# Kernel optimization log

Measured on AMD Instinct MI355X. Metric: run time of the kernel, lower is better.

Reference implementation:

```python
import jax, jax.numpy as jnp
import numpy as np

EPS = 1e-5
HEADS = 16
HEAD_DIM = 64
SIG_SCALE = HEAD_DIM ** (-0.25)
DEFAULT_BIAS = -3.0

def layernorm(x, scale, offset):
    mu = jnp.mean(x, axis=-1, keepdims=True)
    var = jnp.mean(jnp.square(x - mu), axis=-1, keepdims=True)
    return (x - mu) * jax.lax.rsqrt(var + EPS) * scale + offset

def setup_inputs() -> dict:
    key = jax.random.key(0)
    ks = jax.random.split(key, 16)
    B, Nq, Nk, D, A = 2, 2048, 2048, 1024, 1024
    s = 0.02
    return {
        "query_feats": jax.random.normal(ks[0], (B, Nq, D), jnp.float32),
        "key_feats": jax.random.normal(ks[1], (B, Nk, D), jnp.float32),
        "Wq": jax.random.normal(ks[2], (A, D), jnp.float32) * s,
        "Wk": jax.random.normal(ks[3], (A, D), jnp.float32) * s,
        "Wv": jax.random.normal(ks[4], (A, D), jnp.float32) * s,
        "Wo": jax.random.normal(ks[5], (D, A), jnp.float32) * s,
        "qn_scale": jnp.ones((HEAD_DIM,), jnp.float32),
        "qn_bias": jnp.zeros((HEAD_DIM,), jnp.float32),
        "kn_scale": jnp.ones((HEAD_DIM,), jnp.float32),
        "kn_bias": jnp.zeros((HEAD_DIM,), jnp.float32),
        "ln_q_scale": jnp.ones((D,), jnp.float32),
        "ln_q_bias": jnp.zeros((D,), jnp.float32),
        "ln_out_scale": jnp.ones((D,), jnp.float32),
        "ln_out_bias": jnp.zeros((D,), jnp.float32),
        "gamma": jnp.full((D,), 1e-5, jnp.float32),
    }

def reference(query_feats, key_feats, Wq, Wk, Wv, Wo, qn_scale, qn_bias, kn_scale, kn_bias, ln_q_scale, ln_q_bias, ln_out_scale, ln_out_bias, gamma):
    B, Nq, _ = query_feats.shape
    Nk = key_feats.shape[1]
    residual = query_feats
    xq = layernorm(query_feats, ln_q_scale, ln_q_bias)  # norm_first
    # projections (torch Linear: x @ W.T)
    q = (xq @ Wq.T).reshape(B, Nq, HEADS, HEAD_DIM).transpose(0, 2, 1, 3)
    k = (key_feats @ Wk.T).reshape(B, Nk, HEADS, HEAD_DIM).transpose(0, 2, 1, 3)
    v = (key_feats @ Wv.T).reshape(B, Nk, HEADS, HEAD_DIM).transpose(0, 2, 1, 3)
    # qk-norm over head_dim, then fixed sigmoid scale
    q = layernorm(q, qn_scale, qn_bias) * SIG_SCALE
    k = layernorm(k, kn_scale, kn_bias) * SIG_SCALE
    scores = jnp.einsum('bhqd,bhkd->bhqk', q, k) + DEFAULT_BIAS
    # hardware-optimized sigmoid: 0.5*(1+tanh(0.5*x))
    attn = 0.5 * (1.0 + jnp.tanh(0.5 * scores))
    ctx = jnp.einsum('bhqk,bhkd->bhqd', attn, v)
    ctx = ctx.transpose(0, 2, 1, 3).reshape(B, Nq, HEADS * HEAD_DIM)
    out = ctx @ Wo.T
    out = gamma * out
    out = residual + out
    out = layernorm(out, ln_out_scale, ln_out_bias)  # post_norm
    return out
```

## Files before the change

kernel.cpp:

```cpp
#include <hip/hip_runtime.h>

typedef unsigned short u16;
typedef unsigned int u32;
typedef __bf16 bf16x8 __attribute__((ext_vector_type(8)));
typedef float f32x4 __attribute__((ext_vector_type(4)));
typedef float f32x16 __attribute__((ext_vector_type(16)));
typedef u16 u16x8 __attribute__((ext_vector_type(8)));
typedef u16 u16x4 __attribute__((ext_vector_type(4)));
typedef u32 u32x4 __attribute__((ext_vector_type(4)));

#define LN_EPS 1e-5f
#define SIG_SCALE_F 0.35355339059327379f
#define NLOG2E -1.4426950408889634f
#define BIAS_L2E 4.328085122666891f

__device__ __forceinline__ u16 f2bf(float f) {
    u32 u = __builtin_bit_cast(u32, f);
    u32 r = u + 0x7fffu + ((u >> 16) & 1u);
    return (u16)(r >> 16);
}
__device__ __forceinline__ float bf2f(u16 v) {
    return __builtin_bit_cast(float, (u32)v << 16);
}
__device__ __forceinline__ u32 pk_hi(float a, float b) {
    return __builtin_amdgcn_perm(__builtin_bit_cast(u32, b), __builtin_bit_cast(u32, a),
                                 0x07060302u);
}

__device__ __forceinline__ void gload16(const u16* g, u16* lds) {
    __builtin_amdgcn_global_load_lds(
        (const __attribute__((address_space(1))) u32*)g,
        (__attribute__((address_space(3))) u32*)lds, 16, 0, 0);
}

__device__ __forceinline__ void gemm_core(f32x4 acc[4][4],
                                          const u16* __restrict__ A, const u16* __restrict__ B,
                                          int Kiter, int lda, int ldb,
                                          long m0, long n0, u16* As, u16* Bs) {
    const int tid = threadIdx.x;
    const int lane = tid & 63;
    const int wave = tid >> 6;
    const int r15 = lane & 15;
    const int qd = lane >> 4;
    const int wm = (wave >> 1) * 64;
    const int wn = (wave & 1) * 64;

    const int srow = wave * 16 + (lane >> 2);
    const int c0 = (lane & 3) ^ (srow & 3);
    const u16* Ap0 = A + (m0 + srow) * lda + c0 * 8;
    const u16* Ap1 = A + (m0 + srow + 64) * lda + c0 * 8;
    const u16* Bp0 = B + (n0 + srow) * ldb + c0 * 8;
    const u16* Bp1 = B + (n0 + srow + 64) * ldb + c0 * 8;
    u16* As0 = As + wave * 512;
    u16* As1 = As + (wave + 4) * 512;
    u16* Bs0 = Bs + wave * 512;
    u16* Bs1 = Bs + (wave + 4) * 512;

    for (int kt = 0; kt < Kiter; kt += 32) {
        __syncthreads();
        gload16(Ap0 + kt, As0);
        gload16(Ap1 + kt, As1);
        gload16(Bp0 + kt, Bs0);
        gload16(Bp1 + kt, Bs1);
        __syncthreads();
        bf16x8 af[4], bfr[4];
#pragma unroll
        for (int i = 0; i < 4; i++) {
            int row = wm + i * 16 + r15;
            af[i] = *(const bf16x8*)(As + row * 32 + ((qd ^ (row & 3)) * 8));
        }
#pragma unroll
        for (int j = 0; j < 4; j++) {
            int row = wn + j * 16 + r15;
            bfr[j] = *(const bf16x8*)(Bs + row * 32 + ((qd ^ (row & 3)) * 8));
        }
#pragma unroll
        for (int i = 0; i < 4; i++)
#pragma unroll
            for (int j = 0; j < 4; j++)
                acc[i][j] = __builtin_amdgcn_mfma_f32_16x16x32_bf16(af[i], bfr[j], acc[i][j], 0, 0, 0);
    }
}

__global__ __launch_bounds__(256, 3) void gemm_qkv(const u16* __restrict__ xq, const u16* __restrict__ keyb,
                                                   const u16* __restrict__ Wqb, const u16* __restrict__ Wkb,
                                                   const u16* __restrict__ Wvb,
                                                   const float* __restrict__ qns, const float* __restrict__ qnb,
                                                   const float* __restrict__ kns, const float* __restrict__ knb,
                                                   u16* __restrict__ qln, u16* __restrict__ kln,
                                                   u16* __restrict__ vt) {
    __shared__ __attribute__((aligned(16))) u16 As[128 * 32];
    __shared__ __attribute__((aligned(16))) u16 Bs[128 * 32];
    const int z = blockIdx.z;
    const u16* A = (z == 0) ? xq : keyb;
    const u16* B = (z == 0) ? Wqb : ((z == 1) ? Wkb : Wvb);
    const long m0 = (long)blockIdx.x * 128;
    const long n0 = (long)blockIdx.y * 128;

    f32x4 acc[4][4];
#pragma unroll
    for (int i = 0; i < 4; i++)
#pragma unroll
        for (int j = 0; j < 4; j++) acc[i][j] = (f32x4){0.f, 0.f, 0.f, 0.f};

    gemm_core(acc, A, B, 1024, 1024, 1024, m0, n0, As, Bs);

    const int lane = threadIdx.x & 63;
    const int wave = threadIdx.x >> 6;
    const int r15 = lane & 15;
    const int qd = lane >> 4;
    const int wm = (wave >> 1) * 64;
    const int wn = (wave & 1) * 64;

    if (z <= 1) {
        u16* C = (z == 0) ? qln : kln;
        const float* sc_ = (z == 0) ? qns : kns;
        const float* bs_ = (z == 0) ? qnb : knb;
        float scl[4], bia[4];
#pragma unroll
        for (int j = 0; j < 4; j++) {
            scl[j] = sc_[j * 16 + r15] * SIG_SCALE_F;
            bia[j] = bs_[j * 16 + r15] * SIG_SCALE_F;
        }
#pragma unroll
        for (int i = 0; i < 4; i++) {
#pragma unroll
            for (int rr = 0; rr < 4; rr++) {
                float a0 = acc[i][0][rr], a1 = acc[i][1][rr], a2 = acc[i][2][rr], a3 = acc[i][3][rr];
                float s1 = (a0 + a1) + (a2 + a3);
                float s2 = __builtin_fmaf(a3, a3,
                           __builtin_fmaf(a2, a2, __builtin_fmaf(a1, a1, a0 * a0)));
#pragma unroll
                for (int off = 1; off <= 8; off <<= 1) {
                    s1 += __shfl_xor(s1, off, 64);
                    s2 += __shfl_xor(s2, off, 64);
                }
                float mu = s1 * (1.0f / 64.0f);
                float var = __builtin_fmaf(-mu, mu, s2 * (1.0f / 64.0f));
                float rs = rsqrtf(var + LN_EPS);
                long row = m0 + wm + i * 16 + qd * 4 + rr;
#pragma unroll
                for (int j = 0; j < 4; j++) {
                    long col = n0 + wn + j * 16 + r15;
                    float o = __builtin_fmaf((acc[i][j][rr] - mu) * rs, scl[j], bia[j]);
                    C[row * 1024 + col] = f2bf(o);
                }
            }
        }
    } else {
#pragma unroll
        for (int i = 0; i < 4; i++)
#pragma unroll
            for (int rr = 0; rr < 4; rr++) {
                int grow = (int)(m0 + wm + i * 16 + qd * 4 + rr);
                int bb = grow >> 11;
                int kk = grow & 2047;
#pragma unroll
                for (int j = 0; j < 4; j++) {
                    int col = (int)(n0 + wn + j * 16 + r15);
                    int hh = col >> 6;
                    int dd = col & 63;
                    vt[((size_t)(bb * 16 + hh) * 64 + dd) * 2048 + kk] = f2bf(acc[i][j][rr]);
                }
            }
    }
}

__global__ __launch_bounds__(256, 4) void gemm_o(const u16* __restrict__ ctx, const u16* __restrict__ Wob,
                                                 u16* __restrict__ opre) {
    __shared__ __attribute__((aligned(16))) u16 As[128 * 32];
    __shared__ __attribute__((aligned(16))) u16 Bs[128 * 32];
    const int z = blockIdx.z;
    const int koff = z * 256;
    u16* C = opre + (size_t)z * 4194304;
    const long m0 = (long)blockIdx.x * 128;
    const long n0 = (long)blockIdx.y * 128;
    f32x4 acc[4][4];
#pragma unroll
    for (int i = 0; i < 4; i++)
#pragma unroll
        for (int j = 0; j < 4; j++) acc[i][j] = (f32x4){0.f, 0.f, 0.f, 0.f};
    gemm_core(acc, ctx + koff, Wob + koff, 256, 1024, 1024, m0, n0, As, Bs);

    const int lane = threadIdx.x & 63;
    const int wave = threadIdx.x >> 6;
    const int r15 = lane & 15;
    const int qd = lane >> 4;
    const int wm = (wave >> 1) * 64;
    const int wn = (wave & 1) * 64;
#pragma unroll
    for (int i = 0; i < 4; i++)
#pragma unroll
        for (int rr = 0; rr < 4; rr++) {
            long row = m0 + wm + i * 16 + qd * 4 + rr;
#pragma unroll
            for (int j = 0; j < 4; j++)
                C[row * 1024 + n0 + wn + j * 16 + r15] = f2bf(acc[i][j][rr]);
        }
}

__device__ __forceinline__ bf16x8 frag64(const u16* base, int row, int kidx) {
    return *(const bf16x8*)(base + row * 64 + ((kidx ^ (row & 7)) * 8));
}

__global__ __launch_bounds__(512, 4) void attn_sigmoid_v7(const u16* __restrict__ q,
                                                          const u16* __restrict__ k,
                                                          const u16* __restrict__ vt,
                                                          u16* __restrict__ ctx) {
    __shared__ __attribute__((aligned(16))) u16 Sh[8192 + 8192 + 8192];
    u16* Qs = Sh;
    u16* Ks = Sh + 8192;
    u16* Vs = Sh + 16384;
    float* Obuf = (float*)(Sh + 8192);

    const int tid = threadIdx.x;
    const int lane = tid & 63;
    const int wave = tid >> 6;
    const int l31 = lane & 31;
    const int h = lane >> 5;
    const int qsub = wave & 3;
    const int kh = wave >> 2;
    const int hd = blockIdx.x;
    const int q0 = blockIdx.y * 128;
    const int b = blockIdx.z;
    const int bh = b * 16 + hd;

    const int lr0 = lane >> 3;
    const int lc0 = lane & 7;
    {
#pragma unroll
        for (int i = 0; i < 2; i++) {
            int s = wave * 2 + i;
            int row = s * 8 + lr0;
            int c = lc0 ^ (row & 7);
            gload16(q + (size_t)(b * 2048 + q0 + row) * 1024 + hd * 64 + c * 8, Qs + s * 512);
        }
    }
    __syncthreads();
    bf16x8 qB[4];
#pragma unroll
    for (int dblk = 0; dblk < 4; dblk++)
        qB[dblk] = frag64(Qs, qsub * 32 + l31, dblk * 2 + h);

    f32x16 accO[2];
#pragma unroll
    for (int dt = 0; dt < 2; dt++)
#pragma unroll
        for (int r = 0; r < 16; r++) accO[dt][r] = 0.f;

    u16* Ksh = Ks + kh * 4096;
    u16* Vsh = Vs + kh * 4096;
    const int wsub = wave & 3;
    const int kbeg = kh * 1024;
    for (int kc = kbeg; kc < kbeg + 1024; kc += 64) {
        __syncthreads();
#pragma unroll
        for (int i = 0; i < 2; i++) {
            int s = wsub * 2 + i;
            int row = s * 8 + lr0;
            int c = lc0 ^ (row & 7);
            gload16(k + (size_t)(b * 2048 + kc + row) * 1024 + hd * 64 + c * 8, Ksh + s * 512);
            gload16(vt + (size_t)(bh * 64 + row) * 2048 + kc + c * 8, Vsh + s * 512);
        }
        __syncthreads();

        f32x16 accS[2];
#pragma unroll
        for (int mt = 0; mt < 2; mt++) {
#pragma unroll
            for (int r = 0; r < 16; r++) accS[mt][r] = 0.f;
#pragma unroll
            for (int dblk = 0; dblk < 4; dblk++) {
                bf16x8 aK = frag64(Ksh, mt * 32 + l31, dblk * 2 + h);
                accS[mt] = __builtin_amdgcn_mfma_f32_32x32x16_bf16(aK, qB[dblk], accS[mt], 0, 0, 0);
            }
        }

        u32 pg[2][4][2];
#pragma unroll
        for (int mt = 0; mt < 2; mt++)
#pragma unroll
            for (int g = 0; g < 4; g++) {
                float p[4];
#pragma unroll
                for (int e = 0; e < 4; e++) {
                    float t = __builtin_fmaf(accS[mt][g * 4 + e], NLOG2E, BIAS_L2E);
                    float u = __builtin_amdgcn_exp2f(t);
                    p[e] = __builtin_amdgcn_rcpf(1.0f + u);
                }
                pg[mt][g][0] = pk_hi(p[0], p[1]);
                pg[mt][g][1] = pk_hi(p[2], p[3]);
            }

#pragma unroll
        for (int mt = 0; mt < 2; mt++)
#pragma unroll
            for (int kblk = 0; kblk < 2; kblk++) {
                int glo = kblk * 2, ghi = kblk * 2 + 1;
                u32 x0 = (u32)__shfl_xor((int)pg[mt][glo][0], 32, 64);
                u32 x1 = (u32)__shfl_xor((int)pg[mt][glo][1], 32, 64);
                u32 y0 = (u32)__shfl_xor((int)pg[mt][ghi][0], 32, 64);
                u32 y1 = (u32)__shfl_xor((int)pg[mt][ghi][1], 32, 64);
                u32x4 fr;
                fr[0] = h ? y0 : pg[mt][glo][0];
                fr[1] = h ? y1 : pg[mt][glo][1];
                fr[2] = h ? pg[mt][ghi][0] : x0;
                fr[3] = h ? pg[mt][ghi][1] : x1;
                bf16x8 aP = __builtin_bit_cast(bf16x8, fr);
#pragma unroll
                for (int dt = 0; dt < 2; dt++) {
                    bf16x8 bV = frag64(Vsh, dt * 32 + l31, mt * 4 + kblk * 2 + h);
                    accO[dt] = __builtin_amdgcn_mfma_f32_32x32x16_bf16(aP, bV, accO[dt], 0, 0, 0);
                }
            }
    }

    __syncthreads();
    if (kh == 1) {
#pragma unroll
        for (int dt = 0; dt < 2; dt++)
#pragma unroll
            for (int r = 0; r < 16; r++) {
                int ql = qsub * 32 + (r & 3) + 8 * (r >> 2) + 4 * h;
                Obuf[ql * 64 + dt * 32 + l31] = accO[dt][r];
            }
    }
    __syncthreads();
    if (kh == 0) {
#pragma unroll
        for (int dt = 0; dt < 2; dt++)
#pragma unroll
            for (int r = 0; r < 16; r++) {
                int ql = qsub * 32 + (r & 3) + 8 * (r >> 2) + 4 * h;
                float s = accO[dt][r] + Obuf[ql * 64 + dt * 32 + l31];
                ctx[(size_t)(b * 2048 + q0 + ql) * 1024 + hd * 64 + dt * 32 + l31] = f2bf(s);
            }
    }
}

__global__ __launch_bounds__(256) void prep(const float* __restrict__ w0, const float* __restrict__ w1,
                                            const float* __restrict__ w2, const float* __restrict__ w3,
                                            const float* __restrict__ kf, const float* __restrict__ qf,
                                            const float* __restrict__ lnq_s, const float* __restrict__ lnq_b,
                                            u16* __restrict__ wdst, u16* __restrict__ kdst,
                                            u16* __restrict__ xq) {
    const int bx = blockIdx.x;
    const int tid = threadIdx.x;
    if (bx < 6144) {
        size_t e = ((size_t)bx * 256 + tid) * 4;
        const float* src;
        u16* dst;
        if (e < 4194304) {
            src = ((e >> 20) == 0 ? w0 : (e >> 20) == 1 ? w1 : (e >> 20) == 2 ? w2 : w3) + (e & 1048575);
            dst = wdst + e;
        } else {
            size_t off = e - 4194304;
            src = kf + off;
            dst = kdst + off;
        }
        float4 xv = *(const float4*)src;
        u16x4 o;
        o[0] = f2bf(xv.x);
        o[1] = f2bf(xv.y);
        o[2] = f2bf(xv.z);
        o[3] = f2bf(xv.w);
        *(u16x4*)dst = o;
    } else {
        __shared__ float s1buf[4], s2buf[4];
        const int row = bx - 6144;
        const size_t base = (size_t)row * 1024 + tid * 4;
        const float4 xv = *(const float4*)(qf + base);
        float s1 = xv.x + xv.y + xv.z + xv.w;
        float s2 = xv.x * xv.x + xv.y * xv.y + xv.z * xv.z + xv.w * xv.w;
        int lane = tid & 63, wave = tid >> 6;
#pragma unroll
        for (int off = 32; off > 0; off >>= 1) {
            s1 += __shfl_down(s1, off, 64);
            s2 += __shfl_down(s2, off, 64);
        }
        if (lane == 0) { s1buf[wave] = s1; s2buf[wave] = s2; }
        __syncthreads();
        s1 = s1buf[0] + s1buf[1] + s1buf[2] + s1buf[3];
        s2 = s2buf[0] + s2buf[1] + s2buf[2] + s2buf[3];
        float mu = s1 * (1.0f / 1024.0f);
        float var = s2 * (1.0f / 1024.0f) - mu * mu;
        float rs = rsqrtf(var + LN_EPS);
        const float4 scv = *(const float4*)(lnq_s + tid * 4);
        const float4 bsv = *(const float4*)(lnq_b + tid * 4);
        u16x4 o;
        o[0] = f2bf((xv.x - mu) * rs * scv.x + bsv.x);
        o[1] = f2bf((xv.y - mu) * rs * scv.y + bsv.y);
        o[2] = f2bf((xv.z - mu) * rs * scv.z + bsv.z);
        o[3] = f2bf((xv.w - mu) * rs * scv.w + bsv.w);
        *(u16x4*)(xq + base) = o;
    }
}

__global__ __launch_bounds__(256) void final_ln(const float* __restrict__ resid,
                                                const u16* __restrict__ opre,
                                                const float* __restrict__ gamma,
                                                const float* __restrict__ sc,
                                                const float* __restrict__ bs,
                                                float* __restrict__ out) {
    __shared__ float s1buf[4], s2buf[4];
    const int row = blockIdx.x;
    const int tid = threadIdx.x;
    const size_t base = (size_t)row * 1024 + tid * 4;
    float4 rv = *(const float4*)(resid + base);
    u16x4 p0 = *(const u16x4*)(opre + base);
    u16x4 p1 = *(const u16x4*)(opre + 4194304 + base);
    u16x4 p2 = *(const u16x4*)(opre + 8388608 + base);
    u16x4 p3 = *(const u16x4*)(opre + 12582912 + base);
    float4 gv = *(const float4*)(gamma + tid * 4);
    float4 xv;
    xv.x = rv.x + gv.x * ((bf2f(p0[0]) + bf2f(p1[0])) + (bf2f(p2[0]) + bf2f(p3[0])));
    xv.y = rv.y + gv.y * ((bf2f(p0[1]) + bf2f(p1[1])) + (bf2f(p2[1]) + bf2f(p3[1])));
    xv.z = rv.z + gv.z * ((bf2f(p0[2]) + bf2f(p1[2])) + (bf2f(p2[2]) + bf2f(p3[2])));
    xv.w = rv.w + gv.w * ((bf2f(p0[3]) + bf2f(p1[3])) + (bf2f(p2[3]) + bf2f(p3[3])));
    float s1 = xv.x + xv.y + xv.z + xv.w;
    float s2 = xv.x * xv.x + xv.y * xv.y + xv.z * xv.z + xv.w * xv.w;
    int lane = tid & 63, wave = tid >> 6;
#pragma unroll
    for (int off = 32; off > 0; off >>= 1) {
        s1 += __shfl_down(s1, off, 64);
        s2 += __shfl_down(s2, off, 64);
    }
    if (lane == 0) { s1buf[wave] = s1; s2buf[wave] = s2; }
    __syncthreads();
    s1 = s1buf[0] + s1buf[1] + s1buf[2] + s1buf[3];
    s2 = s2buf[0] + s2buf[1] + s2buf[2] + s2buf[3];
    float mu = s1 * (1.0f / 1024.0f);
    float var = s2 * (1.0f / 1024.0f) - mu * mu;
    float rs = rsqrtf(var + LN_EPS);
    const float4 scv = *(const float4*)(sc + tid * 4);
    const float4 bsv = *(const float4*)(bs + tid * 4);
    float4 o;
    o.x = (xv.x - mu) * rs * scv.x + bsv.x;
    o.y = (xv.y - mu) * rs * scv.y + bsv.y;
    o.z = (xv.z - mu) * rs * scv.z + bsv.z;
    o.w = (xv.w - mu) * rs * scv.w + bsv.w;
    *(float4*)(out + base) = o;
}

extern "C" void kernel_launch(void* const* d_in, const int* in_sizes, int n_in,
                              void* d_out, int out_size, void* d_ws, size_t ws_size,
                              hipStream_t stream) {
    const float* qf    = (const float*)d_in[0];
    const float* kf    = (const float*)d_in[1];
    const float* Wq    = (const float*)d_in[2];
    const float* Wk    = (const float*)d_in[3];
    const float* Wv    = (const float*)d_in[4];
    const float* Wo    = (const float*)d_in[5];
    const float* qn_s  = (const float*)d_in[6];
    const float* qn_b  = (const float*)d_in[7];
    const float* kn_s  = (const float*)d_in[8];
    const float* kn_b  = (const float*)d_in[9];
    const float* lnq_s = (const float*)d_in[10];
    const float* lnq_b = (const float*)d_in[11];
    const float* lno_s = (const float*)d_in[12];
    const float* lno_b = (const float*)d_in[13];
    const float* gamma = (const float*)d_in[14];
    float* out = (float*)d_out;

    char* ws = (char*)d_ws;
    const size_t MB = 1024 * 1024;
    u16* Wqb   = (u16*)(ws + 0 * MB);
    u16* Wkb   = (u16*)(ws + 2 * MB);
    u16* Wvb   = (u16*)(ws + 4 * MB);
    u16* Wob   = (u16*)(ws + 6 * MB);
    u16* xq    = (u16*)(ws + 8 * MB);
    u16* ctx   = (u16*)(ws + 8 * MB);
    u16* keyb  = (u16*)(ws + 16 * MB);
    u16* qln   = (u16*)(ws + 24 * MB);
    u16* kln   = (u16*)(ws + 32 * MB);
    u16* vt    = (u16*)(ws + 48 * MB);
    u16* opre  = (u16*)(ws + 24 * MB);

    prep<<<dim3(10240), 256, 0, stream>>>(Wq, Wk, Wv, Wo, kf, qf, lnq_s, lnq_b, Wqb, keyb, xq);

    gemm_qkv<<<dim3(32, 8, 3), 256, 0, stream>>>(xq, keyb, Wqb, Wkb, Wvb,
                                                 qn_s, qn_b, kn_s, kn_b, qln, kln, vt);

    attn_sigmoid_v7<<<dim3(16, 16, 2), 512, 0, stream>>>(qln, kln, vt, ctx);

    gemm_o<<<dim3(32, 8, 4), 256, 0, stream>>>(ctx, Wob, opre);
    final_ln<<<dim3(4096), 256, 0, stream>>>(qf, opre, gamma, lno_s, lno_b, out);
}
```

Measured before the change: 233.5 us.

## Double-buffer K/V tiles in sigmoid attention and use permlane32 swap

The attention kernel now keeps two shared-memory buffers for K and V. The next 64-key tile is prefetched while the current one is used for MFMA work, and the barrier count per iteration drops from two to one. It also raises wave priority around the MFMA sections with s_setprio. The shfl_xor-plus-select exchange of the P fragments between half-waves is replaced by permlane32_swap. In exchange, LDS per block grows from 48KB to 80KB, which may reduce how many blocks fit on each CU.

```diff
diff --git a/kernel.cpp b/kernel.cpp
--- a/kernel.cpp
+++ b/kernel.cpp
@@ -7,6 +7,7 @@
 typedef float f32x16 __attribute__((ext_vector_type(16)));
 typedef u16 u16x8 __attribute__((ext_vector_type(8)));
 typedef u16 u16x4 __attribute__((ext_vector_type(4)));
+typedef u32 u32x2 __attribute__((ext_vector_type(2)));
 typedef u32 u32x4 __attribute__((ext_vector_type(4)));
 
 #define LN_EPS 1e-5f
@@ -203,14 +204,14 @@
     return *(const bf16x8*)(base + row * 64 + ((kidx ^ (row & 7)) * 8));
 }
 
-__global__ __launch_bounds__(512, 4) void attn_sigmoid_v7(const u16* __restrict__ q,
+__global__ __launch_bounds__(512, 4) void attn_sigmoid_v8(const u16* __restrict__ q,
                                                           const u16* __restrict__ k,
                                                           const u16* __restrict__ vt,
                                                           u16* __restrict__ ctx) {
-    __shared__ __attribute__((aligned(16))) u16 Sh[8192 + 8192 + 8192];
+    __shared__ __attribute__((aligned(16))) u16 Sh[8192 + 16384 + 16384];
     u16* Qs = Sh;
     u16* Ks = Sh + 8192;
-    u16* Vs = Sh + 16384;
+    u16* Vs = Sh + 8192 + 16384;
     float* Obuf = (float*)(Sh + 8192);
 
     const int tid = threadIdx.x;
@@ -227,6 +228,22 @@
 
     const int lr0 = lane >> 3;
     const int lc0 = lane & 7;
+    const int wsub = wave & 3;
+    const int kbeg = kh * 1024;
+
+    auto stageKV = [&](int cur, int kc) {
+#pragma unroll
+        for (int i = 0; i < 2; i++) {
+            int s = wsub * 2 + i;
+            int row = s * 8 + lr0;
+            int c = lc0 ^ (row & 7);
+            gload16(k + (size_t)(b * 2048 + kc + row) * 1024 + hd * 64 + c * 8,
+                    Ks + (cur * 2 + kh) * 4096 + s * 512);
+            gload16(vt + (size_t)(bh * 64 + row) * 2048 + kc + c * 8,
+                    Vs + (cur * 2 + kh) * 4096 + s * 512);
+        }
+    };
+
     {
 #pragma unroll
         for (int i = 0; i < 2; i++) {
@@ -235,6 +252,7 @@
             int c = lc0 ^ (row & 7);
             gload16(q + (size_t)(b * 2048 + q0 + row) * 1024 + hd * 64 + c * 8, Qs + s * 512);
         }
+        stageKV(0, kbeg);
     }
     __syncthreads();
     bf16x8 qB[4];
@@ -248,23 +266,15 @@
 #pragma unroll
         for (int r = 0; r < 16; r++) accO[dt][r] = 0.f;
 
-    u16* Ksh = Ks + kh * 4096;
-    u16* Vsh = Vs + kh * 4096;
-    const int wsub = wave & 3;
-    const int kbeg = kh * 1024;
-    for (int kc = kbeg; kc < kbeg + 1024; kc += 64) {
-        __syncthreads();
-#pragma unroll
-        for (int i = 0; i < 2; i++) {
-            int s = wsub * 2 + i;
-            int row = s * 8 + lr0;
-            int c = lc0 ^ (row & 7);
-            gload16(k + (size_t)(b * 2048 + kc + row) * 1024 + hd * 64 + c * 8, Ksh + s * 512);
-            gload16(vt + (size_t)(bh * 64 + row) * 2048 + kc + c * 8, Vsh + s * 512);
-        }
-        __syncthreads();
+    int cur = 0;
+    for (int it = 0; it < 16; ++it) {
+        const int kc = kbeg + it * 64;
+        if (it < 15) stageKV(cur ^ 1, kc + 64);
+        const u16* Ksh = Ks + (cur * 2 + kh) * 4096;
+        const u16* Vsh = Vs + (cur * 2 + kh) * 4096;
 
         f32x16 accS[2];
+        __builtin_amdgcn_s_setprio(1);
 #pragma unroll
         for (int mt = 0; mt < 2; mt++) {
 #pragma unroll
@@ -275,6 +285,7 @@
                 accS[mt] = __builtin_amdgcn_mfma_f32_32x32x16_bf16(aK, qB[dblk], accS[mt], 0, 0, 0);
             }
         }
+        __builtin_amdgcn_s_setprio(0);
 
         u32 pg[2][4][2];
 #pragma unroll
@@ -292,20 +303,19 @@
                 pg[mt][g][1] = pk_hi(p[2], p[3]);
             }
 
+        __builtin_amdgcn_s_setprio(1);
 #pragma unroll
         for (int mt = 0; mt < 2; mt++)
 #pragma unroll
             for (int kblk = 0; kblk < 2; kblk++) {
                 int glo = kblk * 2, ghi = kblk * 2 + 1;
-                u32 x0 = (u32)__shfl_xor((int)pg[mt][glo][0], 32, 64);
-                u32 x1 = (u32)__shfl_xor((int)pg[mt][glo][1], 32, 64);
-                u32 y0 = (u32)__shfl_xor((int)pg[mt][ghi][0], 32, 64);
-                u32 y1 = (u32)__shfl_xor((int)pg[mt][ghi][1], 32, 64);
+                u32x2 r0 = __builtin_amdgcn_permlane32_swap(pg[mt][glo][0], pg[mt][ghi][0], false, false);
+                u32x2 r1 = __builtin_amdgcn_permlane32_swap(pg[mt][glo][1], pg[mt][ghi][1], false, false);
                 u32x4 fr;
-                fr[0] = h ? y0 : pg[mt][glo][0];
-                fr[1] = h ? y1 : pg[mt][glo][1];
-                fr[2] = h ? pg[mt][ghi][0] : x0;
-                fr[3] = h ? pg[mt][ghi][1] : x1;
+                fr[0] = r0[0];
+                fr[1] = r1[0];
+                fr[2] = r0[1];
+                fr[3] = r1[1];
                 bf16x8 aP = __builtin_bit_cast(bf16x8, fr);
 #pragma unroll
                 for (int dt = 0; dt < 2; dt++) {
@@ -313,9 +323,12 @@
                     accO[dt] = __builtin_amdgcn_mfma_f32_32x32x16_bf16(aP, bV, accO[dt], 0, 0, 0);
                 }
             }
-    }
-
-    __syncthreads();
+        __builtin_amdgcn_s_setprio(0);
+
+        __syncthreads();
+        cur ^= 1;
+    }
+
     if (kh == 1) {
 #pragma unroll
         for (int dt = 0; dt < 2; dt++)
@@ -481,7 +494,7 @@
     gemm_qkv<<<dim3(32, 8, 3), 256, 0, stream>>>(xq, keyb, Wqb, Wkb, Wvb,
                                                  qn_s, qn_b, kn_s, kn_b, qln, kln, vt);
 
-    attn_sigmoid_v7<<<dim3(16, 16, 2), 512, 0, stream>>>(qln, kln, vt, ctx);
+    attn_sigmoid_v8<<<dim3(16, 16, 2), 512, 0, stream>>>(qln, kln, vt, ctx);
 
     gemm_o<<<dim3(32, 8, 4), 256, 0, stream>>>(ctx, Wob, opre);
     final_ln<<<dim3(4096), 256, 0, stream>>>(qf, opre, gamma, lno_s, lno_b, out);
```

Result: faster. 227.3 us (-2.6%).
